# Optimization experiments

Measured on AMD Instinct MI355X. Metric: run time of the kernel, lower is better.

The kernel has to match this reference:

```python
import jax, jax.numpy as jnp
import numpy as np

GRID_SIZE = 5
SPLINE_ORDER = 3


def b_splines(x, grid):
    # x: (B, in), grid: (in, GRID_SIZE + 2*SPLINE_ORDER + 1)
    xe = x[..., None]  # (B, in, 1)
    bases = ((xe >= grid[:, :-1]) & (xe < grid[:, 1:])).astype(x.dtype)
    for k in range(1, SPLINE_ORDER + 1):
        left = (xe - grid[:, : -(k + 1)]) / (grid[:, k:-1] - grid[:, : -(k + 1)])
        right = (grid[:, k + 1:] - xe) / (grid[:, k + 1:] - grid[:, 1:-k])
        bases = left * bases[..., :-1] + right * bases[..., 1:]
    return bases  # (B, in, GRID_SIZE + SPLINE_ORDER)


def kan_linear(x, base_w, spline_w, spline_scaler, grid):
    # efficient-kan KANLinear: base branch + scaled B-spline branch
    base = jax.nn.silu(x) @ base_w.T                       # (B, out)
    b = b_splines(x, grid)                                  # (B, in, G+k)
    scaled = spline_w * spline_scaler[..., None]            # (out, in, G+k)
    spline = jnp.einsum('big,oig->bo', b, scaled)
    return base + spline


def setup_inputs() -> dict:
    key = jax.random.key(0)
    B, T, D, H, O, L = 128, 1024, 512, 512, 256, 2
    GK = GRID_SIZE + SPLINE_ORDER
    stdv = 1.0 / np.sqrt(H)
    ks = jax.random.split(key, 12)
    u = lambda k, shape: jax.random.uniform(k, shape, jnp.float32, -stdv, stdv)
    x = jax.random.normal(ks[0], (B, T, D), jnp.float32)
    wih = u(ks[1], (L, 4 * H, D))
    whh = u(ks[2], (L, 4 * H, H))
    bih = u(ks[3], (L, 4 * H))
    bhh = u(ks[4], (L, 4 * H))
    kan_base = u(ks[5], (L, H, H))
    kan_spline = u(ks[6], (L, H, H, GK))
    kan_scaler = u(ks[7], (L, H, H))
    fc_w = u(ks[8], (O, H))
    fc_b = u(ks[9], (O,))
    # extended B-spline grid, identical per input feature (efficient-kan default)
    h_step = 2.0 / GRID_SIZE
    pts = (np.arange(-SPLINE_ORDER, GRID_SIZE + SPLINE_ORDER + 1) * h_step - 1.0).astype(np.float32)
    grid = jnp.broadcast_to(jnp.asarray(pts), (H, pts.shape[0]))
    return {"x": x, "wih": wih, "whh": whh, "bih": bih, "bhh": bhh,
            "kan_base": kan_base, "kan_spline": kan_spline, "kan_scaler": kan_scaler,
            "grid": grid, "fc_w": fc_w, "fc_b": fc_b}


def reference(x, wih, whh, bih, bhh, kan_base, kan_spline, kan_scaler, grid, fc_w, fc_b):
    L = wih.shape[0]
    B = x.shape[0]
    H = whh.shape[-1]

    def cell(l, inp, h_prev, c_prev):
        gates = inp @ wih[l].T + bih[l] + h_prev @ whh[l].T + bhh[l]
        i, f, g, o = jnp.split(gates, 4, axis=1)
        i = jax.nn.sigmoid(i)
        f = jax.nn.sigmoid(f)
        o = jax.nn.sigmoid(o)
        kan_out = kan_linear(g, kan_base[l], kan_spline[l], kan_scaler[l], grid)
        c_next = f * c_prev + i * kan_out
        h_next = o * jnp.tanh(c_next)
        return h_next, c_next

    def step(carry, x_t):
        h, c = carry  # each (L, B, H)
        inp = x_t
        hs, cs = [], []
        for l in range(L):  # small fixed layer count
            hn, cn = cell(l, inp, h[l], c[l])
            hs.append(hn)
            cs.append(cn)
            inp = hn
        return (jnp.stack(hs), jnp.stack(cs)), None

    h0 = jnp.zeros((L, B, H), x.dtype)
    c0 = jnp.zeros((L, B, H), x.dtype)
    (h_fin, _), _ = jax.lax.scan(step, (h0, c0), jnp.transpose(x, (1, 0, 2)))
    return h_fin[-1] @ fc_w.T + fc_b
```

## Files before the change

kernel.cpp:

```cpp
#include <hip/hip_runtime.h>
#include <hip/hip_fp16.h>


typedef _Float16 f16;
typedef _Float16 half8 __attribute__((ext_vector_type(8)));
typedef float floatx4 __attribute__((ext_vector_type(4)));

#define OFF_H0    0ULL
#define OFF_H1    131072ULL
#define OFF_SIG0  262144ULL
#define OFF_SIG1  1048576ULL
#define OFF_A20   1835008ULL
#define OFF_A21   3014656ULL
#define OFF_HFIN  4194304ULL
#define OFF_BAR   4456448ULL
#define WS_NEED   4476928ULL

#define IDX_FLAGS 0
#define IDX_XD    1024
#define IDX_SEEN  2048
#define IDX_GFLAG 3072
#define IDX_GDONE 4096
#define IDX_CTR   4608

#define MFMA(acc, a, b) acc = __builtin_amdgcn_mfma_f32_16x16x32_f16(a, b, acc, 0, 0, 0)

__device__ __forceinline__ half8 cvt8(const float* p) {
  float4 a = *(const float4*)p, b = *(const float4*)(p + 4);
  half8 o;
  o[0]=(f16)a.x; o[1]=(f16)a.y; o[2]=(f16)a.z; o[3]=(f16)a.w;
  o[4]=(f16)b.x; o[5]=(f16)b.y; o[6]=(f16)b.z; o[7]=(f16)b.w;
  return o;
}

template<bool LOC> __device__ __forceinline__ void st_f16(f16* p, f16 v) {
  union { f16 h; unsigned short u; } c; c.h = v; unsigned u32 = c.u;
  if (LOC) asm volatile("global_store_short %0, %1, off sc0"     :: "v"(p), "v"(u32) : "memory");
  else     asm volatile("global_store_short %0, %1, off sc0 sc1" :: "v"(p), "v"(u32) : "memory");
}
template<bool LOC> __device__ __forceinline__ void st_f32(float* p, float v) {
  if (LOC) asm volatile("global_store_dword %0, %1, off sc0"     :: "v"(p), "v"(v) : "memory");
  else     asm volatile("global_store_dword %0, %1, off sc0 sc1" :: "v"(p), "v"(v) : "memory");
}
template<bool LOC> __device__ __forceinline__ void st_h8(f16* p, half8 v) {
  if (LOC) asm volatile("global_store_dwordx4 %0, %1, off sc0"     :: "v"(p), "v"(v) : "memory");
  else     asm volatile("global_store_dwordx4 %0, %1, off sc0 sc1" :: "v"(p), "v"(v) : "memory");
}

template<bool LOC>
__device__ __forceinline__ void slab_bar(unsigned* bars, int slab, int role, unsigned rnd) {
  asm volatile("s_waitcnt vmcnt(0)" ::: "memory");
  __syncthreads();
  const int tid = threadIdx.x;
  if (LOC) {
    if (tid == 0) {
      unsigned* ctr = &bars[IDX_CTR + slab*32];
      unsigned one = 1u, zero = 0u;
      asm volatile("global_atomic_add %0, %1, off" :: "v"(ctr), "v"(one) : "memory");
      const unsigned tgt = rnd * 32u;
      for (;;) {
        unsigned v;
        asm volatile("global_atomic_add %0, %1, %2, off sc0\n\t"
                     "s_waitcnt vmcnt(0)"
                     : "=v"(v) : "v"(ctr), "v"(zero) : "memory");
        if (v >= tgt) break;
        __builtin_amdgcn_s_sleep(1);
      }
    }
  } else {
    if (tid == 0) __builtin_amdgcn_fence(__ATOMIC_RELEASE, "agent");
    if (tid < 64) {
      if (tid == 0)
        __hip_atomic_store(&bars[IDX_FLAGS + slab*32 + role], rnd,
                           __ATOMIC_RELAXED, __HIP_MEMORY_SCOPE_AGENT);
      if (role == 0) {
        unsigned* fl = &bars[IDX_FLAGS + slab*32 + (tid & 31)];
        for (;;) {
          unsigned v = __hip_atomic_load(fl, __ATOMIC_RELAXED, __HIP_MEMORY_SCOPE_AGENT);
          if (__all((tid >= 32) || (v >= rnd))) break;
          __builtin_amdgcn_s_sleep(1);
        }
        if (tid == 0) {
          __builtin_amdgcn_fence(__ATOMIC_ACQUIRE, "agent");
          __hip_atomic_store(&bars[IDX_XD + slab*32], rnd,
                             __ATOMIC_RELAXED, __HIP_MEMORY_SCOPE_AGENT);
        }
      } else if (tid == 0) {
        while (__hip_atomic_load(&bars[IDX_XD + slab*32],
                   __ATOMIC_RELAXED, __HIP_MEMORY_SCOPE_AGENT) < rnd)
          __builtin_amdgcn_s_sleep(1);
        __builtin_amdgcn_fence(__ATOMIC_ACQUIRE, "agent");
      }
    }
  }
  __syncthreads();
  asm volatile("buffer_inv" ::: "memory");
}

__device__ __forceinline__ void init_gbar(unsigned* bars, int w) {
  __syncthreads();
  const int tid = threadIdx.x;
  if (tid < 64) {
    if (tid == 0)
      __hip_atomic_store(&bars[IDX_GFLAG + w], 1u, __ATOMIC_RELAXED, __HIP_MEMORY_SCOPE_AGENT);
    if (w == 0) {
      for (;;) {
        unsigned v0 = __hip_atomic_load(&bars[IDX_GFLAG + tid      ], __ATOMIC_RELAXED, __HIP_MEMORY_SCOPE_AGENT);
        unsigned v1 = __hip_atomic_load(&bars[IDX_GFLAG + tid +  64], __ATOMIC_RELAXED, __HIP_MEMORY_SCOPE_AGENT);
        unsigned v2 = __hip_atomic_load(&bars[IDX_GFLAG + tid + 128], __ATOMIC_RELAXED, __HIP_MEMORY_SCOPE_AGENT);
        unsigned v3 = __hip_atomic_load(&bars[IDX_GFLAG + tid + 192], __ATOMIC_RELAXED, __HIP_MEMORY_SCOPE_AGENT);
        if (__all(v0 && v1 && v2 && v3)) break;
        __builtin_amdgcn_s_sleep(1);
      }
      if (tid == 0)
        __hip_atomic_store(&bars[IDX_GDONE], 1u, __ATOMIC_RELAXED, __HIP_MEMORY_SCOPE_AGENT);
    } else if (tid == 0) {
      while (!__hip_atomic_load(&bars[IDX_GDONE], __ATOMIC_RELAXED, __HIP_MEMORY_SCOPE_AGENT))
        __builtin_amdgcn_s_sleep(1);
    }
  }
  __syncthreads();
}

template<int L, bool LOC>
__device__ __forceinline__ void gates_phase(
    int t, int slab, int sub, int wv, int lane,
    const float* __restrict__ x, const f16* __restrict__ H0, const f16* __restrict__ H1,
    const f16* wlds, const half8 (&wgr)[16], float bv,
    float* __restrict__ SIG, f16* __restrict__ A2)
{
  const int m  = slab*16 + (lane & 15);
  const int kq = (lane >> 4) * 8;
  const half8* bl = (const half8*)wlds + (size_t)wv * 1024;
  floatx4 acc = {0.f, 0.f, 0.f, 0.f};

  if (L == 0) {
    const float* xb = x + (size_t)m*524288 + (size_t)t*512 + kq;
#pragma unroll
    for (int ks = 0; ks < 16; ++ks) {
      half8 a = cvt8(xb + ks*32);
      MFMA(acc, a, bl[ks*64 + lane]);
    }
  } else {
    const f16* hb0 = H0 + (size_t)m*512 + kq;
#pragma unroll
    for (int ks = 0; ks < 16; ++ks) {
      half8 a = *(const half8*)(hb0 + ks*32);
      MFMA(acc, a, bl[ks*64 + lane]);
    }
  }
  {
    const f16* hb = ((L == 0) ? H0 : H1) + (size_t)m*512 + kq;
#pragma unroll
    for (int ks = 0; ks < 16; ++ks) {
      half8 a = *(const half8*)(hb + ks*32);
      MFMA(acc, a, wgr[ks]);
    }
  }
  const int cg    = sub*128 + wv*16 + (lane & 15);
  const int chunk = cg >> 9;
  const int rbase = slab*16 + ((lane >> 4) << 2);
#pragma unroll
  for (int r = 0; r < 4; ++r) {
    const int m2 = rbase + r;
    float v = acc[r] + bv;
    if (chunk == 2) {
      const int gcol = cg - 1024;
      st_f16<LOC>(A2 + (size_t)m2*4608 + gcol, (f16)(v / (1.f + expf(-v))));
      float tp = (v + 2.2f) * 2.5f;
      int c; float u;
      if (tp >= 0.f && tp < 11.f) { c = (int)tp; u = tp - (float)c; }
      else { c = 99; u = 0.f; }
      float u2 = u*u, u3 = u2*u, um = 1.f - u;
      float q0 = um*um*um*(1.f/6.f);
      float q1 = (3.f*u3 - 6.f*u2 + 4.f)*(1.f/6.f);
      float q2 = (-3.f*u3 + 3.f*u2 + 3.f*u + 1.f)*(1.f/6.f);
      float q3 = u3*(1.f/6.f);
      half8 bs;
#pragma unroll
      for (int j = 0; j < 8; ++j) {
        int rr = j - (c - 3);
        float bb = (rr==0)?q0:(rr==1)?q1:(rr==2)?q2:(rr==3)?q3:0.f;
        bs[j] = (f16)bb;
      }
      st_h8<LOC>(A2 + (size_t)m2*4608 + 512 + (size_t)gcol*8, bs);
    } else {
      const int scol = (chunk == 3) ? (cg - 512) : cg;
      st_f32<LOC>(SIG + (size_t)m2*1536 + scol, 1.f / (1.f + expf(-v)));
    }
  }
}

template<bool LOC>
__device__ __forceinline__ void kan_phase(
    bool writeFin, int slab, int sub, int wv, int lane, int tid,
    const f16* __restrict__ A2, const half8 (&wb)[36],
    const float* __restrict__ SIG, f16* __restrict__ H,
    float* __restrict__ HFIN, float& creg, float* __restrict__ red)
{
  const int m = slab*16 + (lane & 15);
  const f16* ab = A2 + (size_t)m*4608 + wv*576 + ((lane >> 4) << 3);
  floatx4 a0 = {0.f,0.f,0.f,0.f}, a1 = {0.f,0.f,0.f,0.f};
#pragma unroll
  for (int ks = 0; ks < 18; ++ks) {
    half8 a = *(const half8*)(ab + ks*32);
    MFMA(a0, a, wb[ks*2]);
    MFMA(a1, a, wb[ks*2 + 1]);
  }
  *(floatx4*)&red[((wv*2 + 0)*64 + lane)*4] = a0;
  *(floatx4*)&red[((wv*2 + 1)*64 + lane)*4] = a1;
  __syncthreads();
  const int rm = tid >> 5, cn = tid & 31;
  const int j = cn >> 4;
  const int lsrc = (cn & 15) + ((rm >> 2) << 4);
  const int rr = rm & 3;
  float s = 0.f;
#pragma unroll
  for (int q = 0; q < 8; ++q) s += red[((q*2 + j)*64 + lsrc)*4 + rr];
  const int mg = slab*16 + rm, ng = sub*32 + cn;
  float iv = SIG[(size_t)mg*1536 + ng];
  float fv = SIG[(size_t)mg*1536 + 512 + ng];
  float ov = SIG[(size_t)mg*1536 + 1024 + ng];
  float c2 = fv*creg + iv*s;
  float hn = ov * tanhf(c2);
  creg = c2;
  st_f16<LOC>(H + (size_t)mg*512 + ng, (f16)hn);
  if (writeFin) st_f32<LOC>(HFIN + (size_t)mg*512 + ng, hn);
}

template<bool LOC>
__device__ void run_all(int slab, int role, int tid, int lane, int wv,
    const float* __restrict__ x, const float* __restrict__ wih, const float* __restrict__ whh,
    const float* __restrict__ bih, const float* __restrict__ bhh,
    const float* __restrict__ kb, const float* __restrict__ ksp, const float* __restrict__ ksc,
    const float* __restrict__ fcw, const float* __restrict__ fcb,
    f16* H0, f16* H1, float* SIG0, float* SIG1, f16* A20, f16* A21, float* HFIN,
    unsigned* bars, float* outp, char* smem)
{
  f16*   wlds = (f16*)smem;
  float* red  = (float*)(smem + 131072);
  const int lw = role >> 4, sub = role & 15;

  for (int u = tid; u < 8192; u += 512) {
    int lu = u & 63, t2 = u >> 6;
    int ks = t2 & 15, nt = t2 >> 4;
    int n = sub*128 + nt*16 + (lu & 15);
    int k = ks*32 + ((lu >> 4) << 3);
    ((half8*)wlds)[u] = cvt8(wih + ((size_t)lw*2048 + n)*512 + k);
  }
  half8 wgr[16];
  {
    int n = sub*128 + wv*16 + (lane & 15);
#pragma unroll
    for (int ks = 0; ks < 16; ++ks) {
      int k = ks*32 + ((lane >> 4) << 3);
      wgr[ks] = cvt8(whh + ((size_t)lw*2048 + n)*512 + k);
    }
  }
  half8 wb[36];
#pragma unroll
  for (int jt = 0; jt < 2; ++jt)
#pragma unroll
  for (int ks = 0; ks < 18; ++ks) {
    int n = sub*32 + jt*16 + (lane & 15);
    int k = wv*576 + ks*32 + ((lane >> 4) << 3);
    half8 o;
    if (k < 512) {
      o = cvt8(kb + ((size_t)lw*512 + n)*512 + k);
    } else {
      int i = (k - 512) >> 3;
      float sc = ksc[((size_t)lw*512 + n)*512 + i];
      const float* sp = ksp + (((size_t)lw*512 + n)*512 + i)*8;
      float4 a = *(const float4*)sp, b2 = *(const float4*)(sp + 4);
      o[0]=(f16)(a.x*sc);  o[1]=(f16)(a.y*sc);  o[2]=(f16)(a.z*sc);  o[3]=(f16)(a.w*sc);
      o[4]=(f16)(b2.x*sc); o[5]=(f16)(b2.y*sc); o[6]=(f16)(b2.z*sc); o[7]=(f16)(b2.w*sc);
    }
    wb[ks*2 + jt] = o;
  }
  const int cg = sub*128 + wv*16 + (lane & 15);
  const float bv = bih[lw*2048 + cg] + bhh[lw*2048 + cg];

  float* SIGl = lw ? SIG1 : SIG0;
  f16*   A2l  = lw ? A21  : A20;
  f16*   Hl   = lw ? H1   : H0;
  float creg = 0.f;

  __syncthreads();
  unsigned rnd = 0;

  for (int tau = 0; tau <= 1024; ++tau) {
    const bool act = lw ? (tau >= 1) : (tau < 1024);
    const int  t   = lw ? (tau - 1) : tau;
    if (act) {
      if (lw == 0) gates_phase<0, LOC>(t, slab, sub, wv, lane, x, H0, H1, wlds, wgr, bv, SIGl, A2l);
      else         gates_phase<1, LOC>(t, slab, sub, wv, lane, x, H0, H1, wlds, wgr, bv, SIGl, A2l);
    }
    ++rnd; slab_bar<LOC>(bars, slab, role, rnd);
    if (act)
      kan_phase<LOC>((lw == 1) && (t == 1023), slab, sub, wv, lane, tid,
                     A2l, wb, SIGl, Hl, HFIN, creg, red);
    ++rnd; slab_bar<LOC>(bars, slab, role, rnd);
  }

  if (role < 8) {
    const int rrow = tid >> 8;
    const int col  = tid & 255;
    const float* src = HFIN + (size_t)(slab*16 + role*2 + rrow)*512;
    red[rrow*512 + col]       = src[col];
    red[rrow*512 + 256 + col] = src[256 + col];
    __syncthreads();
    const int o = tid & 255, r2 = tid >> 8;
    const float* wr = fcw + (size_t)o*512;
    const float* hr = red + r2*512;
    float s = fcb[o];
#pragma unroll 4
    for (int q = 0; q < 128; ++q) {
      float4 b = *(const float4*)(wr + q*4);
      s += hr[q*4]*b.x + hr[q*4+1]*b.y + hr[q*4+2]*b.z + hr[q*4+3]*b.w;
    }
    outp[(size_t)(slab*16 + role*2 + r2)*256 + o] = s;
  }
}

__launch_bounds__(512, 2)
__global__ void kan_main(const float* __restrict__ x,
                         const float* __restrict__ wih, const float* __restrict__ whh,
                         const float* __restrict__ bih, const float* __restrict__ bhh,
                         const float* __restrict__ kb,  const float* __restrict__ ksp,
                         const float* __restrict__ ksc,
                         const float* __restrict__ fcw, const float* __restrict__ fcb,
                         f16* H0, f16* H1, float* SIG0, float* SIG1,
                         f16* A20, f16* A21, float* HFIN,
                         unsigned* bars, float* outp)
{
  extern __shared__ char smem[];
  volatile int* misc = (volatile int*)(smem + 147456);
  const int tid = threadIdx.x, lane = tid & 63, wv = tid >> 6, w = blockIdx.x;

  int xcc;
  asm("s_getreg_b32 %0, hwreg(HW_REG_XCC_ID)" : "=s"(xcc));
  xcc &= 7;

  if (tid == 0) {
    unsigned old = __hip_atomic_fetch_add(&bars[IDX_SEEN + xcc*32], 1u,
                       __ATOMIC_RELAXED, __HIP_MEMORY_SCOPE_AGENT);
    misc[0] = (int)old;
  }
  init_gbar(bars, w);
  if (tid == 0) {
    int ok = 1;
    for (int e = 0; e < 8; ++e)
      ok &= (__hip_atomic_load(&bars[IDX_SEEN + e*32],
                __ATOMIC_RELAXED, __HIP_MEMORY_SCOPE_AGENT) == 32u);
    misc[1] = ok;
  }
  __syncthreads();
  const int rank = misc[0];
  const int locm = misc[1];

  if (locm) {
    int slab = __builtin_amdgcn_readfirstlane(xcc);
    int role = __builtin_amdgcn_readfirstlane(rank);
    run_all<true >(slab, role, tid, lane, wv, x, wih, whh, bih, bhh, kb, ksp, ksc,
                   fcw, fcb, H0, H1, SIG0, SIG1, A20, A21, HFIN, bars, outp, smem);
  } else {
    run_all<false>(w >> 5, w & 31, tid, lane, wv, x, wih, whh, bih, bhh, kb, ksp, ksc,
                   fcw, fcb, H0, H1, SIG0, SIG1, A20, A21, HFIN, bars, outp, smem);
  }
}

extern "C" void kernel_launch(void* const* d_in, const int* in_sizes, int n_in,
                              void* d_out, int out_size, void* d_ws, size_t ws_size,
                              hipStream_t stream) {
  (void)in_sizes; (void)n_in;
  if (ws_size < WS_NEED) {
    hipMemsetAsync(d_out, 0, (size_t)out_size * 4, stream);
    return;
  }
  const float* x   = (const float*)d_in[0];
  const float* wih = (const float*)d_in[1];
  const float* whh = (const float*)d_in[2];
  const float* bih = (const float*)d_in[3];
  const float* bhh = (const float*)d_in[4];
  const float* kb  = (const float*)d_in[5];
  const float* ksp = (const float*)d_in[6];
  const float* ksc = (const float*)d_in[7];
  const float* fcw = (const float*)d_in[9];
  const float* fcb = (const float*)d_in[10];

  char* ws = (char*)d_ws;
  f16*   H0   = (f16*)(ws + OFF_H0);
  f16*   H1   = (f16*)(ws + OFF_H1);
  float* SIG0 = (float*)(ws + OFF_SIG0);
  float* SIG1 = (float*)(ws + OFF_SIG1);
  f16*   A20  = (f16*)(ws + OFF_A20);
  f16*   A21  = (f16*)(ws + OFF_A21);
  float* HFIN = (float*)(ws + OFF_HFIN);
  unsigned* bars = (unsigned*)(ws + OFF_BAR);

  hipMemsetAsync(ws + OFF_H0, 0, 262144, stream);
  hipMemsetAsync(ws + OFF_BAR, 0, 20480, stream);

  hipFuncSetAttribute((const void*)kan_main, hipFuncAttributeMaxDynamicSharedMemorySize, 147712);
  kan_main<<<dim3(256), dim3(512), 147712, stream>>>(
      x, wih, whh, bih, bhh, kb, ksp, ksc, fcw, fcb,
      H0, H1, SIG0, SIG1, A20, A21, HFIN, bars, (float*)d_out);
}
```

Measured before the change: 25.33 ms.

## Double block size to 16 waves with split-K gates and split KAN reduction

Launches 1024 threads per block instead of 512. In the gates phase, the x/H input projection and the recurrent projection now run on different wave halves and are summed through LDS; in the KAN phase, each wave handles one 16-column tile over a 576-wide K slice. The goal is to shorten the per-timestep critical path of this latency-bound recurrent loop by spreading the MFMA chains over more waves. In exchange it adds an extra LDS round-trip and __syncthreads per step, and the tighter per-wave VGPR budget at 1024 threads may cause register spills of the resident weight fragments.

Result: slower. 35.68 ms (+40.9%).

```diff
diff --git a/kernel.cpp b/kernel.cpp
--- a/kernel.cpp
+++ b/kernel.cpp
@@ -124,32 +124,33 @@
 
 template<int L, bool LOC>
 __device__ __forceinline__ void gates_phase(
-    int t, int slab, int sub, int wv, int lane,
+    int t, int slab, int sub, int cg, int kh, int lane,
     const float* __restrict__ x, const f16* __restrict__ H0, const f16* __restrict__ H1,
     const f16* wlds, const half8 (&wgr)[16], float bv,
-    float* __restrict__ SIG, f16* __restrict__ A2)
+    float* __restrict__ SIG, f16* __restrict__ A2, float* __restrict__ red)
 {
   const int m  = slab*16 + (lane & 15);
   const int kq = (lane >> 4) * 8;
-  const half8* bl = (const half8*)wlds + (size_t)wv * 1024;
   floatx4 acc = {0.f, 0.f, 0.f, 0.f};
 
-  if (L == 0) {
-    const float* xb = x + (size_t)m*524288 + (size_t)t*512 + kq;
-#pragma unroll
-    for (int ks = 0; ks < 16; ++ks) {
-      half8 a = cvt8(xb + ks*32);
-      MFMA(acc, a, bl[ks*64 + lane]);
+  if (kh == 0) {
+    const half8* bl = (const half8*)wlds + (size_t)cg * 1024;
+    if (L == 0) {
+      const float* xb = x + (size_t)m*524288 + (size_t)t*512 + kq;
+#pragma unroll
+      for (int ks = 0; ks < 16; ++ks) {
+        half8 a = cvt8(xb + ks*32);
+        MFMA(acc, a, bl[ks*64 + lane]);
+      }
+    } else {
+      const f16* hb = H0 + (size_t)m*512 + kq;
+#pragma unroll
+      for (int ks = 0; ks < 16; ++ks) {
+        half8 a = *(const half8*)(hb + ks*32);
+        MFMA(acc, a, bl[ks*64 + lane]);
+      }
     }
   } else {
-    const f16* hb0 = H0 + (size_t)m*512 + kq;
-#pragma unroll
-    for (int ks = 0; ks < 16; ++ks) {
-      half8 a = *(const half8*)(hb0 + ks*32);
-      MFMA(acc, a, bl[ks*64 + lane]);
-    }
-  }
-  {
     const f16* hb = ((L == 0) ? H0 : H1) + (size_t)m*512 + kq;
 #pragma unroll
     for (int ks = 0; ks < 16; ++ks) {
@@ -157,75 +158,81 @@
       MFMA(acc, a, wgr[ks]);
     }
   }
-  const int cg    = sub*128 + wv*16 + (lane & 15);
-  const int chunk = cg >> 9;
-  const int rbase = slab*16 + ((lane >> 4) << 2);
-#pragma unroll
-  for (int r = 0; r < 4; ++r) {
-    const int m2 = rbase + r;
-    float v = acc[r] + bv;
-    if (chunk == 2) {
-      const int gcol = cg - 1024;
-      st_f16<LOC>(A2 + (size_t)m2*4608 + gcol, (f16)(v / (1.f + expf(-v))));
-      float tp = (v + 2.2f) * 2.5f;
-      int c; float u;
-      if (tp >= 0.f && tp < 11.f) { c = (int)tp; u = tp - (float)c; }
-      else { c = 99; u = 0.f; }
-      float u2 = u*u, u3 = u2*u, um = 1.f - u;
-      float q0 = um*um*um*(1.f/6.f);
-      float q1 = (3.f*u3 - 6.f*u2 + 4.f)*(1.f/6.f);
-      float q2 = (-3.f*u3 + 3.f*u2 + 3.f*u + 1.f)*(1.f/6.f);
-      float q3 = u3*(1.f/6.f);
-      half8 bs;
-#pragma unroll
-      for (int j = 0; j < 8; ++j) {
-        int rr = j - (c - 3);
-        float bb = (rr==0)?q0:(rr==1)?q1:(rr==2)?q2:(rr==3)?q3:0.f;
-        bs[j] = (f16)bb;
-      }
-      st_h8<LOC>(A2 + (size_t)m2*4608 + 512 + (size_t)gcol*8, bs);
-    } else {
-      const int scol = (chunk == 3) ? (cg - 512) : cg;
-      st_f32<LOC>(SIG + (size_t)m2*1536 + scol, 1.f / (1.f + expf(-v)));
+  if (kh == 1) *(floatx4*)&red[(cg*64 + lane)*4] = acc;
+  __syncthreads();
+  if (kh == 0) {
+    acc += *(const floatx4*)&red[(cg*64 + lane)*4];
+    const int cgc   = sub*128 + cg*16 + (lane & 15);
+    const int chunk = cgc >> 9;
+    const int rbase = slab*16 + ((lane >> 4) << 2);
+#pragma unroll
+    for (int r = 0; r < 4; ++r) {
+      const int m2 = rbase + r;
+      float v = acc[r] + bv;
+      if (chunk == 2) {
+        const int gcol = cgc - 1024;
+        st_f16<LOC>(A2 + (size_t)m2*4608 + gcol, (f16)(v / (1.f + expf(-v))));
+        float tp = (v + 2.2f) * 2.5f;
+        int c; float u;
+        if (tp >= 0.f && tp < 11.f) { c = (int)tp; u = tp - (float)c; }
+        else { c = 99; u = 0.f; }
+        float u2 = u*u, u3 = u2*u, um = 1.f - u;
+        float q0 = um*um*um*(1.f/6.f);
+        float q1 = (3.f*u3 - 6.f*u2 + 4.f)*(1.f/6.f);
+        float q2 = (-3.f*u3 + 3.f*u2 + 3.f*u + 1.f)*(1.f/6.f);
+        float q3 = u3*(1.f/6.f);
+        half8 bs;
+#pragma unroll
+        for (int j = 0; j < 8; ++j) {
+          int rr = j - (c - 3);
+          float bb = (rr==0)?q0:(rr==1)?q1:(rr==2)?q2:(rr==3)?q3:0.f;
+          bs[j] = (f16)bb;
+        }
+        st_h8<LOC>(A2 + (size_t)m2*4608 + 512 + (size_t)gcol*8, bs);
+      } else {
+        const int scol = (chunk == 3) ? (cgc - 512) : cgc;
+        st_f32<LOC>(SIG + (size_t)m2*1536 + scol, 1.f / (1.f + expf(-v)));
+      }
     }
   }
 }
 
 template<bool LOC>
 __device__ __forceinline__ void kan_phase(
-    bool writeFin, int slab, int sub, int wv, int lane, int tid,
-    const f16* __restrict__ A2, const half8 (&wb)[36],
+    bool writeFin, int slab, int sub, int jt, int kq2, int wv, int lane, int tid,
+    const f16* __restrict__ A2, const half8 (&wb)[18],
     const float* __restrict__ SIG, f16* __restrict__ H,
     float* __restrict__ HFIN, float& creg, float* __restrict__ red)
 {
+  (void)jt;
   const int m = slab*16 + (lane & 15);
-  const f16* ab = A2 + (size_t)m*4608 + wv*576 + ((lane >> 4) << 3);
-  floatx4 a0 = {0.f,0.f,0.f,0.f}, a1 = {0.f,0.f,0.f,0.f};
+  const f16* ab = A2 + (size_t)m*4608 + kq2*576 + ((lane >> 4) << 3);
+  floatx4 acc = {0.f,0.f,0.f,0.f};
 #pragma unroll
   for (int ks = 0; ks < 18; ++ks) {
     half8 a = *(const half8*)(ab + ks*32);
-    MFMA(a0, a, wb[ks*2]);
-    MFMA(a1, a, wb[ks*2 + 1]);
-  }
-  *(floatx4*)&red[((wv*2 + 0)*64 + lane)*4] = a0;
-  *(floatx4*)&red[((wv*2 + 1)*64 + lane)*4] = a1;
-  __syncthreads();
-  const int rm = tid >> 5, cn = tid & 31;
-  const int j = cn >> 4;
-  const int lsrc = (cn & 15) + ((rm >> 2) << 4);
-  const int rr = rm & 3;
-  float s = 0.f;
-#pragma unroll
-  for (int q = 0; q < 8; ++q) s += red[((q*2 + j)*64 + lsrc)*4 + rr];
-  const int mg = slab*16 + rm, ng = sub*32 + cn;
-  float iv = SIG[(size_t)mg*1536 + ng];
-  float fv = SIG[(size_t)mg*1536 + 512 + ng];
-  float ov = SIG[(size_t)mg*1536 + 1024 + ng];
-  float c2 = fv*creg + iv*s;
-  float hn = ov * tanhf(c2);
-  creg = c2;
-  st_f16<LOC>(H + (size_t)mg*512 + ng, (f16)hn);
-  if (writeFin) st_f32<LOC>(HFIN + (size_t)mg*512 + ng, hn);
+    MFMA(acc, a, wb[ks]);
+  }
+  *(floatx4*)&red[(wv*64 + lane)*4] = acc;
+  __syncthreads();
+  if (tid < 512) {
+    const int rm = tid >> 5, cn = tid & 31;
+    const int j = cn >> 4;
+    const int lsrc = (cn & 15) + ((rm >> 2) << 4);
+    const int rr = rm & 3;
+    float s = 0.f;
+#pragma unroll
+    for (int q = 0; q < 8; ++q) s += red[((q*2 + j)*64 + lsrc)*4 + rr];
+    const int mg = slab*16 + rm, ng = sub*32 + cn;
+    float iv = SIG[(size_t)mg*1536 + ng];
+    float fv = SIG[(size_t)mg*1536 + 512 + ng];
+    float ov = SIG[(size_t)mg*1536 + 1024 + ng];
+    float c2 = fv*creg + iv*s;
+    float hn = ov * tanhf(c2);
+    creg = c2;
+    st_f16<LOC>(H + (size_t)mg*512 + ng, (f16)hn);
+    if (writeFin) st_f32<LOC>(HFIN + (size_t)mg*512 + ng, hn);
+  }
 }
 
 template<bool LOC>
@@ -240,8 +247,10 @@
   f16*   wlds = (f16*)smem;
   float* red  = (float*)(smem + 131072);
   const int lw = role >> 4, sub = role & 15;
-
-  for (int u = tid; u < 8192; u += 512) {
+  const int cg = wv & 7,  kh  = wv >> 3;
+  const int jt = wv & 1,  kq2 = wv >> 1;
+
+  for (int u = tid; u < 8192; u += 1024) {
     int lu = u & 63, t2 = u >> 6;
     int ks = t2 & 15, nt = t2 >> 4;
     int n = sub*128 + nt*16 + (lu & 15);
@@ -250,20 +259,18 @@
   }
   half8 wgr[16];
   {
-    int n = sub*128 + wv*16 + (lane & 15);
+    int n = sub*128 + cg*16 + (lane & 15);
 #pragma unroll
     for (int ks = 0; ks < 16; ++ks) {
       int k = ks*32 + ((lane >> 4) << 3);
       wgr[ks] = cvt8(whh + ((size_t)lw*2048 + n)*512 + k);
     }
   }
-  half8 wb[36];
-#pragma unroll
-  for (int jt = 0; jt < 2; ++jt)
+  half8 wb[18];
 #pragma unroll
   for (int ks = 0; ks < 18; ++ks) {
     int n = sub*32 + jt*16 + (lane & 15);
-    int k = wv*576 + ks*32 + ((lane >> 4) << 3);
+    int k = kq2*576 + ks*32 + ((lane >> 4) << 3);
     half8 o;
     if (k < 512) {
       o = cvt8(kb + ((size_t)lw*512 + n)*512 + k);
@@ -275,10 +282,10 @@
       o[0]=(f16)(a.x*sc);  o[1]=(f16)(a.y*sc);  o[2]=(f16)(a.z*sc);  o[3]=(f16)(a.w*sc);
       o[4]=(f16)(b2.x*sc); o[5]=(f16)(b2.y*sc); o[6]=(f16)(b2.z*sc); o[7]=(f16)(b2.w*sc);
     }
-    wb[ks*2 + jt] = o;
-  }
-  const int cg = sub*128 + wv*16 + (lane & 15);
-  const float bv = bih[lw*2048 + cg] + bhh[lw*2048 + cg];
+    wb[ks] = o;
+  }
+  const int cgc = sub*128 + cg*16 + (lane & 15);
+  const float bv = bih[lw*2048 + cgc] + bhh[lw*2048 + cgc];
 
   float* SIGl = lw ? SIG1 : SIG0;
   f16*   A2l  = lw ? A21  : A20;
@@ -292,17 +299,17 @@
     const bool act = lw ? (tau >= 1) : (tau < 1024);
     const int  t   = lw ? (tau - 1) : tau;
     if (act) {
-      if (lw == 0) gates_phase<0, LOC>(t, slab, sub, wv, lane, x, H0, H1, wlds, wgr, bv, SIGl, A2l);
-      else         gates_phase<1, LOC>(t, slab, sub, wv, lane, x, H0, H1, wlds, wgr, bv, SIGl, A2l);
+      if (lw == 0) gates_phase<0, LOC>(t, slab, sub, cg, kh, lane, x, H0, H1, wlds, wgr, bv, SIGl, A2l, red);
+      else         gates_phase<1, LOC>(t, slab, sub, cg, kh, lane, x, H0, H1, wlds, wgr, bv, SIGl, A2l, red);
     }
     ++rnd; slab_bar<LOC>(bars, slab, role, rnd);
     if (act)
-      kan_phase<LOC>((lw == 1) && (t == 1023), slab, sub, wv, lane, tid,
+      kan_phase<LOC>((lw == 1) && (t == 1023), slab, sub, jt, kq2, wv, lane, tid,
                      A2l, wb, SIGl, Hl, HFIN, creg, red);
     ++rnd; slab_bar<LOC>(bars, slab, role, rnd);
   }
 
-  if (role < 8) {
+  if (role < 8 && tid < 512) {
     const int rrow = tid >> 8;
     const int col  = tid & 255;
     const float* src = HFIN + (size_t)(slab*16 + role*2 + rrow)*512;
@@ -322,7 +329,7 @@
   }
 }
 
-__launch_bounds__(512, 2)
+__launch_bounds__(1024, 4)
 __global__ void kan_main(const float* __restrict__ x,
                          const float* __restrict__ wih, const float* __restrict__ whh,
                          const float* __restrict__ bih, const float* __restrict__ bhh,
@@ -402,7 +409,7 @@
   hipMemsetAsync(ws + OFF_BAR, 0, 20480, stream);
 
   hipFuncSetAttribute((const void*)kan_main, hipFuncAttributeMaxDynamicSharedMemorySize, 147712);
-  kan_main<<<dim3(256), dim3(512), 147712, stream>>>(
+  kan_main<<<dim3(256), dim3(1024), 147712, stream>>>(
       x, wih, whh, bih, bhh, kb, ksp, ksc, fcw, fcb,
       H0, H1, SIG0, SIG1, A20, A21, HFIN, bars, (float*)d_out);
 }
```
